# Performance work log

Hardware: AMD Instinct MI355X
Metric: run time of the kernel (lower is better)

## Reference

```python
import jax, jax.numpy as jnp
import numpy as np

L = 8        # num_coupling
W = 128      # MLP hidden width
B = 262144   # batch size


def _lin(k, out_d, in_d):
    # torch nn.Linear default init: U(-1/sqrt(in_d), 1/sqrt(in_d))
    scale = 1.0 / np.sqrt(in_d)
    kw, kb = jax.random.split(k)
    Wm = jax.random.uniform(kw, (L, out_d, in_d), minval=-scale, maxval=scale, dtype=jnp.float32)
    bm = jax.random.uniform(kb, (L, out_d), minval=-scale, maxval=scale, dtype=jnp.float32)
    return Wm, bm


def setup_inputs() -> dict:
    key = jax.random.key(0)
    ks = jax.random.split(key, 10)
    x = jax.random.normal(ks[0], (B, 2), dtype=jnp.float32)
    s_scale = jax.random.normal(ks[1], (L,), dtype=jnp.float32)
    s_W1, s_b1 = _lin(ks[2], W, 1)
    s_W2, s_b2 = _lin(ks[3], W, W)
    s_W3, s_b3 = _lin(ks[4], W, W)
    s_W4, s_b4 = _lin(ks[5], 1, W)
    t_W1, t_b1 = _lin(ks[6], W, 1)
    t_W2, t_b2 = _lin(ks[7], W, W)
    t_W3, t_b3 = _lin(ks[8], W, W)
    t_W4, t_b4 = _lin(ks[9], 1, W)
    return dict(x=x, s_scale=s_scale,
                s_W1=s_W1, s_b1=s_b1, s_W2=s_W2, s_b2=s_b2, s_W3=s_W3, s_b3=s_b3, s_W4=s_W4, s_b4=s_b4,
                t_W1=t_W1, t_b1=t_b1, t_W2=t_W2, t_b2=t_b2, t_W3=t_W3, t_b3=t_b3, t_W4=t_W4, t_b4=t_b4)


def _mlp(z, W1, b1, W2, b2, W3, b3, W4, b4):
    # backbone: Linear->ReLU x3, Linear->Tanh; z: [B,1] -> [B,1]
    h = jax.nn.relu(z @ W1.T + b1)
    h = jax.nn.relu(h @ W2.T + b2)
    h = jax.nn.relu(h @ W3.T + b3)
    return jnp.tanh(h @ W4.T + b4)


def reference(x, s_scale,
              s_W1, s_b1, s_W2, s_b2, s_W3, s_b3, s_W4, s_b4,
              t_W1, t_b1, t_W2, t_b2, t_W3, t_b3, t_W4, t_b4):
    # training-mode forward of NormalizingFlow2D
    a = x[:, :1]
    b = x[:, 1:]
    s_vals = []
    for i in range(L):
        if i % 2 == 0:
            s = s_scale[i] * _mlp(a, s_W1[i], s_b1[i], s_W2[i], s_b2[i], s_W3[i], s_b3[i], s_W4[i], s_b4[i])
            b = jnp.exp(s) * b + _mlp(a, t_W1[i], t_b1[i], t_W2[i], t_b2[i], t_W3[i], t_b3[i], t_W4[i], t_b4[i])
        else:
            s = s_scale[i] * _mlp(b, s_W1[i], s_b1[i], s_W2[i], s_b2[i], s_W3[i], s_b3[i], s_W4[i], s_b4[i])
            a = jnp.exp(s) * a + _mlp(b, t_W1[i], t_b1[i], t_W2[i], t_b2[i], t_W3[i], t_b3[i], t_W4[i], t_b4[i])
        s_vals.append(s)
    out = jnp.concatenate([a, b], axis=1)          # [B, 2]
    s_cat = jnp.concatenate(s_vals, axis=0)        # [L*B, 1]  (torch.cat default dim=0)
    return out, s_cat
```

## Files before the change

### kernel.cpp

```cpp
#include <hip/hip_runtime.h>

#define LNUM 8
#define WD 128
#define BATCH 262144

typedef unsigned int u32;
typedef __attribute__((ext_vector_type(8))) short bf16x8;
typedef __attribute__((ext_vector_type(4))) float f32x4;

__device__ __forceinline__ u32 pk2(float x, float y){
  u32 r;
  asm("v_cvt_pk_bf16_f32 %0, %1, %2" : "=v"(r) : "v"(x), "v"(y));
  return r;
}

__device__ __forceinline__ void fence(){ __builtin_amdgcn_sched_barrier(0); }

__device__ __forceinline__ void stage_Wnat(const float* __restrict__ src, u32* dst, int tid){
  const int j = tid >> 1, h = tid & 1;
  const float* s = src + j * WD + h * 64;
  u32* drow = dst + j * 64;
  const int base = h * 32;
  const u32 sz = (u32)((j & 7) << 2);
#pragma unroll
  for(int c = 0; c < 8; ++c){
    float4 f0 = *(const float4*)(s + c * 8);
    float4 f1 = *(const float4*)(s + c * 8 + 4);
    uint4 w;
    w.x = pk2(f0.x, f0.y); w.y = pk2(f0.z, f0.w);
    w.z = pk2(f1.x, f1.y); w.w = pk2(f1.z, f1.w);
    *(uint4*)(drow + (((u32)(base + c * 4)) ^ sz)) = w;
  }
}

__device__ __forceinline__ void stage_Wperm(const float* __restrict__ src, u32* dst, int tid){
  const int j = tid >> 1, h = tid & 1;
  const float* srow = src + j * WD;
  u32* drow = dst + j * 64;
  const u32 sz = (u32)((j & 7) << 2);
#pragma unroll
  for(int kk = 0; kk < 2; ++kk){
    const int kt = 2 * h + kk;
#pragma unroll
    for(int g = 0; g < 4; ++g){
      float4 f0 = *(const float4*)(srow + kt * 32 + g * 4);
      float4 f1 = *(const float4*)(srow + kt * 32 + 16 + g * 4);
      uint4 w;
      w.x = pk2(f0.x, f0.y); w.y = pk2(f0.z, f0.w);
      w.z = pk2(f1.x, f1.y); w.w = pk2(f1.z, f1.w);
      *(uint4*)(drow + (((u32)(kt * 16 + g * 4)) ^ sz)) = w;
    }
  }
}

__device__ __forceinline__ void stage_dma(const u32* __restrict__ g, u32* l, int wv, int lane){
#pragma unroll
  for(int it = 0; it < 8; ++it){
    const int o = wv * 2048 + it * 256;
    __builtin_amdgcn_global_load_lds(
        (const __attribute__((address_space(1))) u32*)(g + o + lane * 4),
        (__attribute__((address_space(3))) u32*)(l + o),
        16, 0, 0);
  }
}

__device__ __forceinline__ float mlp_full(
    float u, const u32* __restrict__ W2lds, const u32* __restrict__ W3lds,
    const float* __restrict__ W1, const float* __restrict__ b1,
    const float* __restrict__ b2, const float* __restrict__ b3,
    const float* __restrict__ W4, int lm, int lg)
{
  float ust[4];
#pragma unroll
  for(int st = 0; st < 4; ++st) ust[st] = __shfl(u, st * 16 + lm, 64);

  f32x4 acc1[8][4];
#pragma unroll
  for(int jt = 0; jt < 8; ++jt){
    const float4 bb = *(const float4*)(b2 + jt * 16 + lg * 4);
    const f32x4 binit = {bb.x, bb.y, bb.z, bb.w};
#pragma unroll
    for(int st = 0; st < 4; ++st) acc1[jt][st] = binit;
  }

#pragma unroll
  for(int kt = 0; kt < 4; ++kt){
    const int ko = kt * 32 + lg * 8;
    const float4 w1a = *(const float4*)(W1 + ko);
    const float4 w1b = *(const float4*)(W1 + ko + 4);
    const float4 g1a = *(const float4*)(b1 + ko);
    const float4 g1b = *(const float4*)(b1 + ko + 4);
    bf16x8 bv[4];
#pragma unroll
    for(int st = 0; st < 4; ++st){
      const float uv = ust[st];
      uint4 pk;
      pk.x = pk2(fmaxf(fmaf(uv, w1a.x, g1a.x), 0.f), fmaxf(fmaf(uv, w1a.y, g1a.y), 0.f));
      pk.y = pk2(fmaxf(fmaf(uv, w1a.z, g1a.z), 0.f), fmaxf(fmaf(uv, w1a.w, g1a.w), 0.f));
      pk.z = pk2(fmaxf(fmaf(uv, w1b.x, g1b.x), 0.f), fmaxf(fmaf(uv, w1b.y, g1b.y), 0.f));
      pk.w = pk2(fmaxf(fmaf(uv, w1b.z, g1b.z), 0.f), fmaxf(fmaf(uv, w1b.w, g1b.w), 0.f));
      bv[st] = __builtin_bit_cast(bf16x8, pk);
    }
    const u32 kdw = (u32)(kt * 16 + lg * 4);
#pragma unroll
    for(int jt = 0; jt < 8; ++jt){
      const int j = lm + 16 * jt;
      bf16x8 av = __builtin_bit_cast(bf16x8,
          *(const uint4*)(W2lds + j * 64 + (kdw ^ (u32)((j & 7) << 2))));
#pragma unroll
      for(int st = 0; st < 4; ++st)
        acc1[jt][st] = __builtin_amdgcn_mfma_f32_16x16x32_bf16(av, bv[st], acc1[jt][st], 0, 0, 0);
    }
  }
  fence();

  u32 tr[8][4][2];
#pragma unroll
  for(int jt = 0; jt < 8; ++jt)
#pragma unroll
    for(int st = 0; st < 4; ++st){
      tr[jt][st][0] = pk2(fmaxf(acc1[jt][st][0], 0.f), fmaxf(acc1[jt][st][1], 0.f));
      tr[jt][st][1] = pk2(fmaxf(acc1[jt][st][2], 0.f), fmaxf(acc1[jt][st][3], 0.f));
    }
  fence();

  float p0 = 0.f, p1 = 0.f, p2 = 0.f, p3 = 0.f;
#pragma unroll
  for(int jt = 0; jt < 8; ++jt){
    const int j = lm + 16 * jt;
    const u32 sz = (u32)((j & 7) << 2);
    const u32* r = W3lds + j * 64;
    const float4 bc = *(const float4*)(b3 + jt * 16 + lg * 4);
    const f32x4 cinit = {bc.x, bc.y, bc.z, bc.w};
    f32x4 a0 = cinit, a1 = cinit, a2 = cinit, a3 = cinit;
#pragma unroll
    for(int kt = 0; kt < 4; ++kt){
      bf16x8 av = __builtin_bit_cast(bf16x8,
          *(const uint4*)(r + (((u32)(kt * 16 + lg * 4)) ^ sz)));
      uint4 q0; q0.x = tr[2*kt][0][0]; q0.y = tr[2*kt][0][1];
      q0.z = tr[2*kt+1][0][0]; q0.w = tr[2*kt+1][0][1];
      uint4 q1; q1.x = tr[2*kt][1][0]; q1.y = tr[2*kt][1][1];
      q1.z = tr[2*kt+1][1][0]; q1.w = tr[2*kt+1][1][1];
      uint4 q2; q2.x = tr[2*kt][2][0]; q2.y = tr[2*kt][2][1];
      q2.z = tr[2*kt+1][2][0]; q2.w = tr[2*kt+1][2][1];
      uint4 q3; q3.x = tr[2*kt][3][0]; q3.y = tr[2*kt][3][1];
      q3.z = tr[2*kt+1][3][0]; q3.w = tr[2*kt+1][3][1];
      a0 = __builtin_amdgcn_mfma_f32_16x16x32_bf16(av, __builtin_bit_cast(bf16x8, q0), a0, 0, 0, 0);
      a1 = __builtin_amdgcn_mfma_f32_16x16x32_bf16(av, __builtin_bit_cast(bf16x8, q1), a1, 0, 0, 0);
      a2 = __builtin_amdgcn_mfma_f32_16x16x32_bf16(av, __builtin_bit_cast(bf16x8, q2), a2, 0, 0, 0);
      a3 = __builtin_amdgcn_mfma_f32_16x16x32_bf16(av, __builtin_bit_cast(bf16x8, q3), a3, 0, 0, 0);
    }
    const float4 wc = *(const float4*)(W4 + jt * 16 + lg * 4);
    p0 = fmaf(fmaxf(a0[0], 0.f), wc.x, p0); p0 = fmaf(fmaxf(a0[1], 0.f), wc.y, p0);
    p0 = fmaf(fmaxf(a0[2], 0.f), wc.z, p0); p0 = fmaf(fmaxf(a0[3], 0.f), wc.w, p0);
    p1 = fmaf(fmaxf(a1[0], 0.f), wc.x, p1); p1 = fmaf(fmaxf(a1[1], 0.f), wc.y, p1);
    p1 = fmaf(fmaxf(a1[2], 0.f), wc.z, p1); p1 = fmaf(fmaxf(a1[3], 0.f), wc.w, p1);
    p2 = fmaf(fmaxf(a2[0], 0.f), wc.x, p2); p2 = fmaf(fmaxf(a2[1], 0.f), wc.y, p2);
    p2 = fmaf(fmaxf(a2[2], 0.f), wc.z, p2); p2 = fmaf(fmaxf(a2[3], 0.f), wc.w, p2);
    p3 = fmaf(fmaxf(a3[0], 0.f), wc.x, p3); p3 = fmaf(fmaxf(a3[1], 0.f), wc.y, p3);
    p3 = fmaf(fmaxf(a3[2], 0.f), wc.z, p3); p3 = fmaf(fmaxf(a3[3], 0.f), wc.w, p3);
  }
  fence();
  p0 += __shfl_xor(p0, 16, 64); p0 += __shfl_xor(p0, 32, 64);
  p1 += __shfl_xor(p1, 16, 64); p1 += __shfl_xor(p1, 32, 64);
  p2 += __shfl_xor(p2, 16, 64); p2 += __shfl_xor(p2, 32, 64);
  p3 += __shfl_xor(p3, 16, 64); p3 += __shfl_xor(p3, 32, 64);
  return (lg == 0) ? p0 : (lg == 1) ? p1 : (lg == 2) ? p2 : p3;
}

extern "C" __global__ void __launch_bounds__(256)
prep_kernel(const float* __restrict__ sW2, const float* __restrict__ sW3,
            const float* __restrict__ tW2, const float* __restrict__ tW3,
            u32* __restrict__ ws)
{
  const int b = blockIdx.x;
  const int layer = b >> 2, which = b & 3;
  const float* src = (which == 0 ? sW2 : which == 1 ? sW3 : which == 2 ? tW2 : tW3)
                     + layer * (WD * WD);
  u32* dst = ws + b * 8192;
  if(which & 1) stage_Wperm(src, dst, threadIdx.x);
  else          stage_Wnat (src, dst, threadIdx.x);
}

extern "C" __global__ void __launch_bounds__(512)
flow_dma(const float* __restrict__ x, const float* __restrict__ s_scale,
         const float* __restrict__ sW1, const float* __restrict__ sb1,
         const float* __restrict__ sb2, const float* __restrict__ sb3,
         const float* __restrict__ sW4, const float* __restrict__ sb4,
         const float* __restrict__ tW1, const float* __restrict__ tb1,
         const float* __restrict__ tb2, const float* __restrict__ tb3,
         const float* __restrict__ tW4, const float* __restrict__ tb4,
         const u32* __restrict__ wimg, float* __restrict__ out)
{
  __shared__ u32 Wbuf[2][16384];

  const int tid = threadIdx.x;
  const int lane = tid & 63, lg = lane >> 4, lm = lane & 15, wv = tid >> 6;
  const int gs = (int)blockIdx.x * 512 + tid;

  float2 ab = ((const float2*)x)[gs];
  float* scat = out + 2 * BATCH;
  float sv = 0.f;

  stage_dma(wimg, Wbuf[0], wv, lane);

#pragma unroll 1
  for(int ph = 0; ph < 2 * LNUM; ++ph){
    const int i = ph >> 1, isT = ph & 1, parity = i & 1;
    asm volatile("s_waitcnt vmcnt(0)" ::: "memory");
    __syncthreads();
    if(ph < 2 * LNUM - 1)
      stage_dma(wimg + (ph + 1) * 16384, Wbuf[(ph + 1) & 1], wv, lane);

    const int off = i * WD;
    const float u = parity ? ab.y : ab.x;
    const u32* W2l = Wbuf[ph & 1];
    const u32* W3l = Wbuf[ph & 1] + 8192;

    if(!isT){
      float pre = mlp_full(u, W2l, W3l, sW1 + off, sb1 + off,
                           sb2 + off, sb3 + off, sW4 + off, lm, lg) + sb4[i];
      sv = s_scale[i] * tanhf(pre);
      scat[i * BATCH + gs] = sv;
    } else {
      float pre = mlp_full(u, W2l, W3l, tW1 + off, tb1 + off,
                           tb2 + off, tb3 + off, tW4 + off, lm, lg) + tb4[i];
      const float tv = tanhf(pre);
      const float e = expf(sv);
      if(parity) ab.x = e * ab.x + tv; else ab.y = e * ab.y + tv;
    }
  }

  ((float2*)out)[gs] = ab;
}

extern "C" __global__ void __launch_bounds__(256, 2)
flow_fb(const float* __restrict__ x, const float* __restrict__ s_scale,
        const float* __restrict__ sW1, const float* __restrict__ sb1,
        const float* __restrict__ sW2, const float* __restrict__ sb2,
        const float* __restrict__ sW3, const float* __restrict__ sb3,
        const float* __restrict__ sW4, const float* __restrict__ sb4,
        const float* __restrict__ tW1, const float* __restrict__ tb1,
        const float* __restrict__ tW2, const float* __restrict__ tb2,
        const float* __restrict__ tW3, const float* __restrict__ tb3,
        const float* __restrict__ tW4, const float* __restrict__ tb4,
        float* __restrict__ out)
{
  __shared__ u32 Wlds[2][8192];

  const int tid = threadIdx.x;
  const int lane = tid & 63, lg = lane >> 4, lm = lane & 15;
  const int gs = (int)blockIdx.x * 256 + tid;

  float2 ab = ((const float2*)x)[gs];
  float* scat = out + 2 * BATCH;

#pragma unroll 1
  for(int i = 0; i < LNUM; ++i){
    const int parity = i & 1;
    const float sc = s_scale[i];
    const int off = i * WD, offW = i * (WD * WD);

    __syncthreads();
    stage_Wnat (sW2 + offW, Wlds[0], tid);
    stage_Wperm(sW3 + offW, Wlds[1], tid);
    __syncthreads();
    const float u = parity ? ab.y : ab.x;
    float preS = mlp_full(u, Wlds[0], Wlds[1], sW1 + off, sb1 + off,
                          sb2 + off, sb3 + off, sW4 + off, lm, lg) + sb4[i];
    const float sv = sc * tanhf(preS);
    scat[i * BATCH + gs] = sv;

    __syncthreads();
    stage_Wnat (tW2 + offW, Wlds[0], tid);
    stage_Wperm(tW3 + offW, Wlds[1], tid);
    __syncthreads();
    float preT = mlp_full(u, Wlds[0], Wlds[1], tW1 + off, tb1 + off,
                          tb2 + off, tb3 + off, tW4 + off, lm, lg) + tb4[i];
    const float tv = tanhf(preT);
    const float e = expf(sv);
    if(parity) ab.x = e * ab.x + tv; else ab.y = e * ab.y + tv;
  }

  ((float2*)out)[gs] = ab;
}

extern "C" void kernel_launch(void* const* d_in, const int* in_sizes, int n_in,
                              void* d_out, int out_size, void* d_ws, size_t ws_size,
                              hipStream_t stream) {
  (void)in_sizes; (void)n_in; (void)out_size;
  const float* p[18];
  for(int k = 0; k < 18; ++k) p[k] = (const float*)d_in[k];

  const size_t need = (size_t)32 * 8192 * 4;
  if(ws_size >= need){
    u32* ws = (u32*)d_ws;
    hipLaunchKernelGGL(prep_kernel, dim3(32), dim3(256), 0, stream,
                       p[4], p[6], p[12], p[14], ws);
    hipLaunchKernelGGL(flow_dma, dim3(BATCH / 512), dim3(512), 0, stream,
                       p[0], p[1], p[2], p[3], p[5], p[7], p[8], p[9],
                       p[10], p[11], p[13], p[15], p[16], p[17],
                       (const u32*)ws, (float*)d_out);
  } else {
    hipLaunchKernelGGL(flow_fb, dim3(BATCH / 256), dim3(256), 0, stream,
                       p[0], p[1], p[2], p[3], p[4], p[5], p[6], p[7], p[8], p[9],
                       p[10], p[11], p[12], p[13], p[14], p[15], p[16], p[17],
                       (float*)d_out);
  }
}
```

Before: 270.8 us.

## Switch MLP GEMMs to 32x32x16 bf16 MFMA with new LDS swizzle layout

Rewrites the per-sample MLP so each wave runs 32x32x16 bf16 MFMAs instead of 16x16x32, with matching 16-row XOR swizzle and a new permuted weight layout for W3 in the prep kernel. The final W4 dot product is interleaved with the next tile's MFMAs through double-buffered accumulators, and s_setprio is raised around the MFMA bursts. The intent is to cut LDS operand reads and shuffle and reduction overhead per FLOP. In exchange, the larger f32x16 accumulators raise register pressure, which may lower occupancy.

```diff
diff --git a/kernel.cpp b/kernel.cpp
--- a/kernel.cpp
+++ b/kernel.cpp
@@ -6,7 +6,10 @@
 
 typedef unsigned int u32;
 typedef __attribute__((ext_vector_type(8))) short bf16x8;
-typedef __attribute__((ext_vector_type(4))) float f32x4;
+typedef __attribute__((ext_vector_type(16))) float f32x16;
+
+#define MFMA32 __builtin_amdgcn_mfma_f32_32x32x16_bf16
+#define BC8(x) __builtin_bit_cast(bf16x8, x)
 
 __device__ __forceinline__ u32 pk2(float x, float y){
   u32 r;
@@ -14,14 +17,11 @@
   return r;
 }
 
-__device__ __forceinline__ void fence(){ __builtin_amdgcn_sched_barrier(0); }
-
-__device__ __forceinline__ void stage_Wnat(const float* __restrict__ src, u32* dst, int tid){
+__device__ __forceinline__ void stage_Wnat32(const float* __restrict__ src, u32* dst, int tid){
   const int j = tid >> 1, h = tid & 1;
   const float* s = src + j * WD + h * 64;
   u32* drow = dst + j * 64;
-  const int base = h * 32;
-  const u32 sz = (u32)((j & 7) << 2);
+  const u32 sz = (u32)((j & 15) << 2);
 #pragma unroll
   for(int c = 0; c < 8; ++c){
     float4 f0 = *(const float4*)(s + c * 8);
@@ -29,27 +29,30 @@
     uint4 w;
     w.x = pk2(f0.x, f0.y); w.y = pk2(f0.z, f0.w);
     w.z = pk2(f1.x, f1.y); w.w = pk2(f1.z, f1.w);
-    *(uint4*)(drow + (((u32)(base + c * 4)) ^ sz)) = w;
-  }
-}
-
-__device__ __forceinline__ void stage_Wperm(const float* __restrict__ src, u32* dst, int tid){
+    *(uint4*)(drow + (((u32)(h * 32 + c * 4)) ^ sz)) = w;
+  }
+}
+
+__device__ __forceinline__ void stage_Wperm32(const float* __restrict__ src, u32* dst, int tid){
   const int j = tid >> 1, h = tid & 1;
-  const float* srow = src + j * WD;
+  const float* row = src + j * WD;
   u32* drow = dst + j * 64;
-  const u32 sz = (u32)((j & 7) << 2);
-#pragma unroll
-  for(int kk = 0; kk < 2; ++kk){
-    const int kt = 2 * h + kk;
-#pragma unroll
-    for(int g = 0; g < 4; ++g){
-      float4 f0 = *(const float4*)(srow + kt * 32 + g * 4);
-      float4 f1 = *(const float4*)(srow + kt * 32 + 16 + g * 4);
-      uint4 w;
-      w.x = pk2(f0.x, f0.y); w.y = pk2(f0.z, f0.w);
-      w.z = pk2(f1.x, f1.y); w.w = pk2(f1.z, f1.w);
-      *(uint4*)(drow + (((u32)(kt * 16 + g * 4)) ^ sz)) = w;
-    }
+  const u32 sz = (u32)((j & 15) << 2);
+#pragma unroll
+  for(int bb = 0; bb < 2; ++bb){
+    const int b = 2 * h + bb;
+#pragma unroll
+    for(int q = 0; q < 2; ++q)
+#pragma unroll
+      for(int hi2 = 0; hi2 < 2; ++hi2){
+        const int base = 32 * b + 16 * q + 4 * hi2;
+        uint4 w;
+        w.x = pk2(row[base    ], row[base + 1 ]);
+        w.y = pk2(row[base + 2], row[base + 3 ]);
+        w.z = pk2(row[base + 8], row[base + 9 ]);
+        w.w = pk2(row[base +10], row[base + 11]);
+        *(uint4*)(drow + (((u32)((b * 2 + q) * 8 + hi2 * 4)) ^ sz)) = w;
+      }
   }
 }
 
@@ -64,108 +67,131 @@
   }
 }
 
-__device__ __forceinline__ float mlp_full(
+#define LOAD_ROWVEC(dst0, dst1, dst2, dst3, ptr, mt) \
+    const float4 dst0 = *(const float4*)((ptr) + (mt) * 32 + 4 * hi); \
+    const float4 dst1 = *(const float4*)((ptr) + (mt) * 32 + 4 * hi + 8); \
+    const float4 dst2 = *(const float4*)((ptr) + (mt) * 32 + 4 * hi + 16); \
+    const float4 dst3 = *(const float4*)((ptr) + (mt) * 32 + 4 * hi + 24);
+
+#define SET16(bi, q0, q1, q2, q3) do { \
+    bi[0]=q0.x; bi[1]=q0.y; bi[2]=q0.z; bi[3]=q0.w; \
+    bi[4]=q1.x; bi[5]=q1.y; bi[6]=q1.z; bi[7]=q1.w; \
+    bi[8]=q2.x; bi[9]=q2.y; bi[10]=q2.z; bi[11]=q2.w; \
+    bi[12]=q3.x; bi[13]=q3.y; bi[14]=q3.z; bi[15]=q3.w; \
+  } while(0)
+
+#define FOLD32(mt) do { \
+    LOAD_ROWVEC(f0, f1, f2, f3, W4, mt); \
+    float* d0 = ((mt) & 1) ? &pb0 : &pa0; \
+    float* d1 = ((mt) & 1) ? &pb1 : &pa1; \
+    const f32x16 a0_ = aa[(mt)&1][0]; \
+    const f32x16 a1_ = aa[(mt)&1][1]; \
+    *d0 = fmaf(fmaxf(a0_[0],0.f),f0.x,fmaf(fmaxf(a0_[1],0.f),f0.y,fmaf(fmaxf(a0_[2],0.f),f0.z,fmaf(fmaxf(a0_[3],0.f),f0.w,*d0)))); \
+    *d0 = fmaf(fmaxf(a0_[4],0.f),f1.x,fmaf(fmaxf(a0_[5],0.f),f1.y,fmaf(fmaxf(a0_[6],0.f),f1.z,fmaf(fmaxf(a0_[7],0.f),f1.w,*d0)))); \
+    *d0 = fmaf(fmaxf(a0_[8],0.f),f2.x,fmaf(fmaxf(a0_[9],0.f),f2.y,fmaf(fmaxf(a0_[10],0.f),f2.z,fmaf(fmaxf(a0_[11],0.f),f2.w,*d0)))); \
+    *d0 = fmaf(fmaxf(a0_[12],0.f),f3.x,fmaf(fmaxf(a0_[13],0.f),f3.y,fmaf(fmaxf(a0_[14],0.f),f3.z,fmaf(fmaxf(a0_[15],0.f),f3.w,*d0)))); \
+    *d1 = fmaf(fmaxf(a1_[0],0.f),f0.x,fmaf(fmaxf(a1_[1],0.f),f0.y,fmaf(fmaxf(a1_[2],0.f),f0.z,fmaf(fmaxf(a1_[3],0.f),f0.w,*d1)))); \
+    *d1 = fmaf(fmaxf(a1_[4],0.f),f1.x,fmaf(fmaxf(a1_[5],0.f),f1.y,fmaf(fmaxf(a1_[6],0.f),f1.z,fmaf(fmaxf(a1_[7],0.f),f1.w,*d1)))); \
+    *d1 = fmaf(fmaxf(a1_[8],0.f),f2.x,fmaf(fmaxf(a1_[9],0.f),f2.y,fmaf(fmaxf(a1_[10],0.f),f2.z,fmaf(fmaxf(a1_[11],0.f),f2.w,*d1)))); \
+    *d1 = fmaf(fmaxf(a1_[12],0.f),f3.x,fmaf(fmaxf(a1_[13],0.f),f3.y,fmaf(fmaxf(a1_[14],0.f),f3.z,fmaf(fmaxf(a1_[15],0.f),f3.w,*d1)))); \
+  } while(0)
+
+__device__ __forceinline__ float mlp32x32(
     float u, const u32* __restrict__ W2lds, const u32* __restrict__ W3lds,
     const float* __restrict__ W1, const float* __restrict__ b1,
     const float* __restrict__ b2, const float* __restrict__ b3,
-    const float* __restrict__ W4, int lm, int lg)
+    const float* __restrict__ W4, int lane31, int hi, int lane)
 {
-  float ust[4];
-#pragma unroll
-  for(int st = 0; st < 4; ++st) ust[st] = __shfl(u, st * 16 + lm, 64);
-
-  f32x4 acc1[8][4];
-#pragma unroll
-  for(int jt = 0; jt < 8; ++jt){
-    const float4 bb = *(const float4*)(b2 + jt * 16 + lg * 4);
-    const f32x4 binit = {bb.x, bb.y, bb.z, bb.w};
-#pragma unroll
-    for(int st = 0; st < 4; ++st) acc1[jt][st] = binit;
-  }
-
-#pragma unroll
-  for(int kt = 0; kt < 4; ++kt){
-    const int ko = kt * 32 + lg * 8;
-    const float4 w1a = *(const float4*)(W1 + ko);
-    const float4 w1b = *(const float4*)(W1 + ko + 4);
-    const float4 g1a = *(const float4*)(b1 + ko);
-    const float4 g1b = *(const float4*)(b1 + ko + 4);
-    bf16x8 bv[4];
-#pragma unroll
-    for(int st = 0; st < 4; ++st){
-      const float uv = ust[st];
-      uint4 pk;
-      pk.x = pk2(fmaxf(fmaf(uv, w1a.x, g1a.x), 0.f), fmaxf(fmaf(uv, w1a.y, g1a.y), 0.f));
-      pk.y = pk2(fmaxf(fmaf(uv, w1a.z, g1a.z), 0.f), fmaxf(fmaf(uv, w1a.w, g1a.w), 0.f));
-      pk.z = pk2(fmaxf(fmaf(uv, w1b.x, g1b.x), 0.f), fmaxf(fmaf(uv, w1b.y, g1b.y), 0.f));
-      pk.w = pk2(fmaxf(fmaf(uv, w1b.z, g1b.z), 0.f), fmaxf(fmaf(uv, w1b.w, g1b.w), 0.f));
-      bv[st] = __builtin_bit_cast(bf16x8, pk);
+  const float us0 = __shfl(u, lane31, 64);
+  const float us1 = __shfl(u, 32 + lane31, 64);
+
+  f32x16 acc1[4][2];
+#pragma unroll
+  for(int mt = 0; mt < 4; ++mt){
+    LOAD_ROWVEC(q0, q1, q2, q3, b2, mt);
+    f32x16 bi;
+    SET16(bi, q0, q1, q2, q3);
+    acc1[mt][0] = bi; acc1[mt][1] = bi;
+  }
+
+#pragma unroll
+  for(int kt = 0; kt < 8; ++kt){
+    const int kb = kt * 16 + hi * 8;
+    const float4 wa = *(const float4*)(W1 + kb);
+    const float4 wb = *(const float4*)(W1 + kb + 4);
+    const float4 ga = *(const float4*)(b1 + kb);
+    const float4 gb = *(const float4*)(b1 + kb + 4);
+    uint4 bv0, bv1;
+    bv0.x = pk2(fmaxf(fmaf(us0, wa.x, ga.x), 0.f), fmaxf(fmaf(us0, wa.y, ga.y), 0.f));
+    bv0.y = pk2(fmaxf(fmaf(us0, wa.z, ga.z), 0.f), fmaxf(fmaf(us0, wa.w, ga.w), 0.f));
+    bv0.z = pk2(fmaxf(fmaf(us0, wb.x, gb.x), 0.f), fmaxf(fmaf(us0, wb.y, gb.y), 0.f));
+    bv0.w = pk2(fmaxf(fmaf(us0, wb.z, gb.z), 0.f), fmaxf(fmaf(us0, wb.w, gb.w), 0.f));
+    bv1.x = pk2(fmaxf(fmaf(us1, wa.x, ga.x), 0.f), fmaxf(fmaf(us1, wa.y, ga.y), 0.f));
+    bv1.y = pk2(fmaxf(fmaf(us1, wa.z, ga.z), 0.f), fmaxf(fmaf(us1, wa.w, ga.w), 0.f));
+    bv1.z = pk2(fmaxf(fmaf(us1, wb.x, gb.x), 0.f), fmaxf(fmaf(us1, wb.y, gb.y), 0.f));
+    bv1.w = pk2(fmaxf(fmaf(us1, wb.z, gb.z), 0.f), fmaxf(fmaf(us1, wb.w, gb.w), 0.f));
+    __builtin_amdgcn_s_setprio(1);
+#pragma unroll
+    for(int mt = 0; mt < 4; ++mt){
+      const int j = mt * 32 + lane31;
+      const u32 sz = (u32)((j & 15) << 2);
+      bf16x8 av = BC8(*(const uint4*)(W2lds + j * 64 + (((u32)(kt * 8 + hi * 4)) ^ sz)));
+      acc1[mt][0] = MFMA32(av, BC8(bv0), acc1[mt][0], 0, 0, 0);
+      acc1[mt][1] = MFMA32(av, BC8(bv1), acc1[mt][1], 0, 0, 0);
     }
-    const u32 kdw = (u32)(kt * 16 + lg * 4);
-#pragma unroll
-    for(int jt = 0; jt < 8; ++jt){
-      const int j = lm + 16 * jt;
-      bf16x8 av = __builtin_bit_cast(bf16x8,
-          *(const uint4*)(W2lds + j * 64 + (kdw ^ (u32)((j & 7) << 2))));
-#pragma unroll
-      for(int st = 0; st < 4; ++st)
-        acc1[jt][st] = __builtin_amdgcn_mfma_f32_16x16x32_bf16(av, bv[st], acc1[jt][st], 0, 0, 0);
-    }
-  }
-  fence();
-
-  u32 tr[8][4][2];
-#pragma unroll
-  for(int jt = 0; jt < 8; ++jt)
-#pragma unroll
-    for(int st = 0; st < 4; ++st){
-      tr[jt][st][0] = pk2(fmaxf(acc1[jt][st][0], 0.f), fmaxf(acc1[jt][st][1], 0.f));
-      tr[jt][st][1] = pk2(fmaxf(acc1[jt][st][2], 0.f), fmaxf(acc1[jt][st][3], 0.f));
-    }
-  fence();
-
-  float p0 = 0.f, p1 = 0.f, p2 = 0.f, p3 = 0.f;
-#pragma unroll
-  for(int jt = 0; jt < 8; ++jt){
-    const int j = lm + 16 * jt;
-    const u32 sz = (u32)((j & 7) << 2);
-    const u32* r = W3lds + j * 64;
-    const float4 bc = *(const float4*)(b3 + jt * 16 + lg * 4);
-    const f32x4 cinit = {bc.x, bc.y, bc.z, bc.w};
-    f32x4 a0 = cinit, a1 = cinit, a2 = cinit, a3 = cinit;
-#pragma unroll
-    for(int kt = 0; kt < 4; ++kt){
-      bf16x8 av = __builtin_bit_cast(bf16x8,
-          *(const uint4*)(r + (((u32)(kt * 16 + lg * 4)) ^ sz)));
-      uint4 q0; q0.x = tr[2*kt][0][0]; q0.y = tr[2*kt][0][1];
-      q0.z = tr[2*kt+1][0][0]; q0.w = tr[2*kt+1][0][1];
-      uint4 q1; q1.x = tr[2*kt][1][0]; q1.y = tr[2*kt][1][1];
-      q1.z = tr[2*kt+1][1][0]; q1.w = tr[2*kt+1][1][1];
-      uint4 q2; q2.x = tr[2*kt][2][0]; q2.y = tr[2*kt][2][1];
-      q2.z = tr[2*kt+1][2][0]; q2.w = tr[2*kt+1][2][1];
-      uint4 q3; q3.x = tr[2*kt][3][0]; q3.y = tr[2*kt][3][1];
-      q3.z = tr[2*kt+1][3][0]; q3.w = tr[2*kt+1][3][1];
-      a0 = __builtin_amdgcn_mfma_f32_16x16x32_bf16(av, __builtin_bit_cast(bf16x8, q0), a0, 0, 0, 0);
-      a1 = __builtin_amdgcn_mfma_f32_16x16x32_bf16(av, __builtin_bit_cast(bf16x8, q1), a1, 0, 0, 0);
-      a2 = __builtin_amdgcn_mfma_f32_16x16x32_bf16(av, __builtin_bit_cast(bf16x8, q2), a2, 0, 0, 0);
-      a3 = __builtin_amdgcn_mfma_f32_16x16x32_bf16(av, __builtin_bit_cast(bf16x8, q3), a3, 0, 0, 0);
-    }
-    const float4 wc = *(const float4*)(W4 + jt * 16 + lg * 4);
-    p0 = fmaf(fmaxf(a0[0], 0.f), wc.x, p0); p0 = fmaf(fmaxf(a0[1], 0.f), wc.y, p0);
-    p0 = fmaf(fmaxf(a0[2], 0.f), wc.z, p0); p0 = fmaf(fmaxf(a0[3], 0.f), wc.w, p0);
-    p1 = fmaf(fmaxf(a1[0], 0.f), wc.x, p1); p1 = fmaf(fmaxf(a1[1], 0.f), wc.y, p1);
-    p1 = fmaf(fmaxf(a1[2], 0.f), wc.z, p1); p1 = fmaf(fmaxf(a1[3], 0.f), wc.w, p1);
-    p2 = fmaf(fmaxf(a2[0], 0.f), wc.x, p2); p2 = fmaf(fmaxf(a2[1], 0.f), wc.y, p2);
-    p2 = fmaf(fmaxf(a2[2], 0.f), wc.z, p2); p2 = fmaf(fmaxf(a2[3], 0.f), wc.w, p2);
-    p3 = fmaf(fmaxf(a3[0], 0.f), wc.x, p3); p3 = fmaf(fmaxf(a3[1], 0.f), wc.y, p3);
-    p3 = fmaf(fmaxf(a3[2], 0.f), wc.z, p3); p3 = fmaf(fmaxf(a3[3], 0.f), wc.w, p3);
-  }
-  fence();
-  p0 += __shfl_xor(p0, 16, 64); p0 += __shfl_xor(p0, 32, 64);
-  p1 += __shfl_xor(p1, 16, 64); p1 += __shfl_xor(p1, 32, 64);
-  p2 += __shfl_xor(p2, 16, 64); p2 += __shfl_xor(p2, 32, 64);
-  p3 += __shfl_xor(p3, 16, 64); p3 += __shfl_xor(p3, 32, 64);
-  return (lg == 0) ? p0 : (lg == 1) ? p1 : (lg == 2) ? p2 : p3;
+    __builtin_amdgcn_s_setprio(0);
+  }
+
+  uint4 trq[4][2][2];
+#pragma unroll
+  for(int b = 0; b < 4; ++b)
+#pragma unroll
+    for(int nt = 0; nt < 2; ++nt)
+#pragma unroll
+      for(int q = 0; q < 2; ++q){
+        const f32x16 a = acc1[b][nt];
+        uint4 t;
+        t.x = pk2(fmaxf(a[q*8+0], 0.f), fmaxf(a[q*8+1], 0.f));
+        t.y = pk2(fmaxf(a[q*8+2], 0.f), fmaxf(a[q*8+3], 0.f));
+        t.z = pk2(fmaxf(a[q*8+4], 0.f), fmaxf(a[q*8+5], 0.f));
+        t.w = pk2(fmaxf(a[q*8+6], 0.f), fmaxf(a[q*8+7], 0.f));
+        trq[b][nt][q] = t;
+      }
+
+  f32x16 aa[2][2];
+  float pa0 = 0.f, pb0 = 0.f, pa1 = 0.f, pb1 = 0.f;
+#pragma unroll
+  for(int mt = 0; mt < 4; ++mt){
+    const int j2 = mt * 32 + lane31;
+    const u32 sz = (u32)((j2 & 15) << 2);
+    const u32* r = W3lds + j2 * 64;
+    bf16x8 av[8];
+#pragma unroll
+    for(int c = 0; c < 8; ++c)
+      av[c] = BC8(*(const uint4*)(r + (((u32)(c * 8 + hi * 4)) ^ sz)));
+    LOAD_ROWVEC(q0, q1, q2, q3, b3, mt);
+    f32x16 ci;
+    SET16(ci, q0, q1, q2, q3);
+    aa[mt & 1][0] = ci; aa[mt & 1][1] = ci;
+    if(mt == 1) FOLD32(0);
+    if(mt == 2) FOLD32(1);
+    if(mt == 3) FOLD32(2);
+    __builtin_amdgcn_s_setprio(1);
+#pragma unroll
+    for(int b = 0; b < 4; ++b)
+#pragma unroll
+      for(int q = 0; q < 2; ++q){
+        aa[mt & 1][0] = MFMA32(av[b * 2 + q], BC8(trq[b][0][q]), aa[mt & 1][0], 0, 0, 0);
+        aa[mt & 1][1] = MFMA32(av[b * 2 + q], BC8(trq[b][1][q]), aa[mt & 1][1], 0, 0, 0);
+      }
+    __builtin_amdgcn_s_setprio(0);
+  }
+  FOLD32(3);
+
+  float p0 = pa0 + pb0, p1 = pa1 + pb1;
+  p0 += __shfl_xor(p0, 32, 64);
+  p1 += __shfl_xor(p1, 32, 64);
+  return (lane & 32) ? p1 : p0;
 }
 
 extern "C" __global__ void __launch_bounds__(256)
@@ -177,9 +203,9 @@
   const int layer = b >> 2, which = b & 3;
   const float* src = (which == 0 ? sW2 : which == 1 ? sW3 : which == 2 ? tW2 : tW3)
                      + layer * (WD * WD);
-  u32* dst = ws + b * 8192;
-  if(which & 1) stage_Wperm(src, dst, threadIdx.x);
-  else          stage_Wnat (src, dst, threadIdx.x);
+  u32* dst = ws + (size_t)(2 * layer + (which >> 1)) * 16384 + (size_t)(which & 1) * 8192;
+  if(which & 1) stage_Wperm32(src, dst, threadIdx.x);
+  else          stage_Wnat32 (src, dst, threadIdx.x);
 }
 
 extern "C" __global__ void __launch_bounds__(512)
@@ -195,7 +221,7 @@
   __shared__ u32 Wbuf[2][16384];
 
   const int tid = threadIdx.x;
-  const int lane = tid & 63, lg = lane >> 4, lm = lane & 15, wv = tid >> 6;
+  const int lane = tid & 63, lane31 = lane & 31, hi = lane >> 5, wv = tid >> 6;
   const int gs = (int)blockIdx.x * 512 + tid;
 
   float2 ab = ((const float2*)x)[gs];
@@ -210,7 +236,7 @@
     asm volatile("s_waitcnt vmcnt(0)" ::: "memory");
     __syncthreads();
     if(ph < 2 * LNUM - 1)
-      stage_dma(wimg + (ph + 1) * 16384, Wbuf[(ph + 1) & 1], wv, lane);
+      stage_dma(wimg + (size_t)(ph + 1) * 16384, Wbuf[(ph + 1) & 1], wv, lane);
 
     const int off = i * WD;
     const float u = parity ? ab.y : ab.x;
@@ -218,13 +244,13 @@
     const u32* W3l = Wbuf[ph & 1] + 8192;
 
     if(!isT){
-      float pre = mlp_full(u, W2l, W3l, sW1 + off, sb1 + off,
-                           sb2 + off, sb3 + off, sW4 + off, lm, lg) + sb4[i];
+      float pre = mlp32x32(u, W2l, W3l, sW1 + off, sb1 + off,
+                           sb2 + off, sb3 + off, sW4 + off, lane31, hi, lane) + sb4[i];
       sv = s_scale[i] * tanhf(pre);
       scat[i * BATCH + gs] = sv;
     } else {
-      float pre = mlp_full(u, W2l, W3l, tW1 + off, tb1 + off,
-                           tb2 + off, tb3 + off, tW4 + off, lm, lg) + tb4[i];
+      float pre = mlp32x32(u, W2l, W3l, tW1 + off, tb1 + off,
+                           tb2 + off, tb3 + off, tW4 + off, lane31, hi, lane) + tb4[i];
       const float tv = tanhf(pre);
       const float e = expf(sv);
       if(parity) ab.x = e * ab.x + tv; else ab.y = e * ab.y + tv;
@@ -249,7 +275,7 @@
   __shared__ u32 Wlds[2][8192];
 
   const int tid = threadIdx.x;
-  const int lane = tid & 63, lg = lane >> 4, lm = lane & 15;
+  const int lane = tid & 63, lane31 = lane & 31, hi = lane >> 5;
   const int gs = (int)blockIdx.x * 256 + tid;
 
   float2 ab = ((const float2*)x)[gs];
@@ -262,21 +288,21 @@
     const int off = i * WD, offW = i * (WD * WD);
 
     __syncthreads();
-    stage_Wnat (sW2 + offW, Wlds[0], tid);
-    stage_Wperm(sW3 + offW, Wlds[1], tid);
+    stage_Wnat32 (sW2 + offW, Wlds[0], tid);
+    stage_Wperm32(sW3 + offW, Wlds[1], tid);
     __syncthreads();
     const float u = parity ? ab.y : ab.x;
-    float preS = mlp_full(u, Wlds[0], Wlds[1], sW1 + off, sb1 + off,
-                          sb2 + off, sb3 + off, sW4 + off, lm, lg) + sb4[i];
+    float preS = mlp32x32(u, Wlds[0], Wlds[1], sW1 + off, sb1 + off,
+                          sb2 + off, sb3 + off, sW4 + off, lane31, hi, lane) + sb4[i];
     const float sv = sc * tanhf(preS);
     scat[i * BATCH + gs] = sv;
 
     __syncthreads();
-    stage_Wnat (tW2 + offW, Wlds[0], tid);
-    stage_Wperm(tW3 + offW, Wlds[1], tid);
-    __syncthreads();
-    float preT = mlp_full(u, Wlds[0], Wlds[1], tW1 + off, tb1 + off,
-                          tb2 + off, tb3 + off, tW4 + off, lm, lg) + tb4[i];
+    stage_Wnat32 (tW2 + offW, Wlds[0], tid);
+    stage_Wperm32(tW3 + offW, Wlds[1], tid);
+    __syncthreads();
+    float preT = mlp32x32(u, Wlds[0], Wlds[1], tW1 + off, tb1 + off,
+                          tb2 + off, tb3 + off, tW4 + off, lane31, hi, lane) + tb4[i];
     const float tv = tanhf(preT);
     const float e = expf(sv);
     if(parity) ab.x = e * ab.x + tv; else ab.y = e * ab.y + tv;
```

New measurement: 536.9 us. 98.2% more time.
